# Kernel tuning notes

Measured on AMD Instinct MI355X. Metric: run time of the kernel, lower is better.

The kernel has to match this reference:

```python
import jax, jax.numpy as jnp
import numpy as np

V = 17  # number of skeleton joints (hard-coded in the torch module)
NUM_SUBSET = 3

def _dam_mask():
    # Reproduces the Python masking loops: zero block [12:17,12:17] and rows/cols {3,6,7,9,10}
    m = np.ones((V, V), np.float32)
    m[12:17, 12:17] = 0.0
    for j in (3, 6, 7, 9, 10):
        m[j, :] = 0.0
        m[:, j] = 0.0
    return jnp.asarray(m)

def setup_inputs() -> dict:
    key = jax.random.key(0)
    ks = jax.random.split(key, 8)
    N, Cin, Cout, T, G = 64, 64, 64, 256, 8
    return {
        "x": jax.random.normal(ks[0], (N, Cin, T, V), jnp.float32),
        "A_base": jax.random.uniform(ks[1], (NUM_SUBSET, V, V), jnp.float32),  # fixed adjacency buffer
        "DA": 0.01 * jax.random.normal(ks[2], (NUM_SUBSET, G, V, V), jnp.float32),   # DecoupleA param
        "DAM": 0.01 * jax.random.normal(ks[3], (NUM_SUBSET, G, V, V), jnp.float32),  # DecoupleAM param (masked, detached)
        "conv_w": jax.random.normal(ks[4], (NUM_SUBSET * Cout, Cin), jnp.float32) * (2.0 / Cin) ** 0.5,  # 1x1 conv
        "conv_b": jnp.zeros((NUM_SUBSET * Cout,), jnp.float32),
        "se_w": jax.random.normal(ks[5], (3,), jnp.float32) * 0.5,  # conv2_1: Conv1d(1,1,k=3,pad=1,no bias)
        "bn_gamma": jnp.full((Cout,), 1e-6, jnp.float32),  # bn_init(bn, 1e-6)
        "bn_beta": jnp.zeros((Cout,), jnp.float32),
    }

def reference(x, A_base, DA, DAM, conv_w, conv_b, se_w, bn_gamma, bn_beta):
    G = DA.shape[1]
    Cout = bn_gamma.shape[0]
    N, Cin, T, _ = x.shape
    # --- adjacency assembly: A (buffer, broadcast over groups) + DecoupleA + masked DecoupleAM ---
    A = A_base[:, None] + DA + DAM * _dam_mask()              # [3, G, V, V]
    # torch .repeat(1, out//groups, 1, 1) tiles along channel axis; + 0.04 from A_final loop
    A_final = jnp.tile(A, (1, Cout // G, 1, 1)) + 0.04        # [3, Cout, V, V]
    # --- 1x1 conv C_in -> 3*C_out ---
    m = jnp.einsum('nctv,kc->nktv', x, conv_w) + conv_b[None, :, None, None]
    m = m.reshape(N, NUM_SUBSET, Cout, T, V)
    # --- grouped adjacency aggregation (A_final has no batch dependence) ---
    m = jnp.einsum('nkctv,kcvw->nctw', m, A_final)            # [N, Cout, T, V]
    # --- SE-style channel attention: global avg pool -> Conv1d(k=3) over channels -> sigmoid gate ---
    p = m.mean(axis=(2, 3))                                   # [N, Cout]
    pp = jnp.pad(p, ((0, 0), (1, 1)))
    g = se_w[0] * pp[:, :-2] + se_w[1] * pp[:, 1:-1] + se_w[2] * pp[:, 2:]
    q = m + m * jax.nn.sigmoid(g)[:, :, None, None]
    # --- BatchNorm2d (training mode: batch stats over N,T,V) ---
    mu = q.mean(axis=(0, 2, 3), keepdims=True)
    var = q.var(axis=(0, 2, 3), keepdims=True)
    q = bn_gamma[None, :, None, None] * (q - mu) * jax.lax.rsqrt(var + 1e-5) + bn_beta[None, :, None, None]
    # --- residual (down == identity since in_channels == out_channels) and ReLU ---
    return jax.nn.relu(q + x)
```

## Files before the change

### kernel.cpp

```cpp
#include <hip/hip_runtime.h>
#include <math.h>

#define NN 64
#define CIN 64
#define COUT 64
#define TT 256
#define VV 17
#define NSUB 3
#define GG 8

#define WS_MB 0
#define WS_WBF 12288
#define WS_PSUM 18432
#define WS_SSQ 22528
#define WS_ACOEF 0
#define WS_BCOEF 4096
#define M2_BYTE_OFF 131072ull
#define M2F8_NEED (M2_BYTE_OFF + 1ull * 64 * 64 * 256 * 17)

typedef short bh8 __attribute__((ext_vector_type(8)));
typedef float f32x4 __attribute__((ext_vector_type(4)));
typedef float f32x16 __attribute__((ext_vector_type(16)));
typedef unsigned short u16t;

__device__ __forceinline__ unsigned bf16r(float f) {
    unsigned u = __builtin_bit_cast(unsigned, f);
    return (u + 0x7fffu + ((u >> 16) & 1u)) >> 16;
}
__device__ __forceinline__ float bf2f(unsigned us) {
    return __builtin_bit_cast(float, us << 16);
}

__device__ __forceinline__ float mfull(const float* Ab, const float* DA, const float* DAM,
                                       int s, int g, int v, int w) {
    const unsigned bad = (1u << 3) | (1u << 6) | (1u << 7) | (1u << 9) | (1u << 10);
    float mask = ((v >= 12 && w >= 12) || ((bad >> v) & 1) || ((bad >> w) & 1)) ? 0.f : 1.f;
    int src = ((s * GG + g) * VV + v) * VV + w;
    return Ab[(s * VV + v) * VV + w] + DA[src] + DAM[src] * mask + 0.04f;
}

__global__ void gcn_prep(const float* __restrict__ Ab, const float* __restrict__ DA,
                         const float* __restrict__ DAM, const float* __restrict__ convw,
                         float* __restrict__ ws) {
    int t0 = blockIdx.x * 256 + threadIdx.x;
    int stride = gridDim.x * 256;
    u16t* wbf = (u16t*)(ws + WS_WBF);
    for (int i = t0; i < 192 * 64; i += stride) wbf[i] = (u16t)bf16r(convw[i]);
    u16t* mb = (u16t*)(ws + WS_MB);
    for (int i = t0; i < NSUB * GG * 32 * 32; i += stride) {
        int k = i & 31, w = (i >> 5) & 31, g = (i >> 10) & 7, s = i >> 13;
        u16t val = 0;
        if (w < VV && k < VV) val = (u16t)bf16r(mfull(Ab, DA, DAM, s, g, k, w));
        mb[i] = val;
    }
}

template <int F8OUT>
__global__ __launch_bounds__(512, 4) void gcn_pass1(const float* __restrict__ x,
                                                    const float* __restrict__ convb,
                                                    const float* __restrict__ ws,
                                                    float* __restrict__ out,
                                                    unsigned char* __restrict__ m2f8) {
    __shared__ __align__(16) unsigned char smem[73984];
    u16t* xsT = (u16t*)smem;
    u16t* Wl = (u16t*)(smem + 20736);
    u16t* mt = (u16t*)(smem + 48384);

    const int tid = threadIdx.x;
    const int wv = tid >> 6;
    const int l = tid & 63;
    const int c16 = l & 15;
    const int q4 = (l >> 4) & 3;
    const int c32 = l & 31;
    const int hi = l >> 5;
    const int n = blockIdx.x >> 3;

    {
        const unsigned* wsrc = (const unsigned*)(ws + WS_WBF);
        unsigned* wd = (unsigned*)Wl;
        for (int j = tid; j < 192 * 32; j += 512) wd[(j >> 5) * 36 + (j & 31)] = wsrc[j];
        unsigned* mz = (unsigned*)mt;
        for (int j = tid; j < 6400; j += 512) mz[j] = 0u;
    }

    const u16t* mb16 = (const u16t*)(ws + WS_MB);
    const int madj = (wv * 32 + c32) * 32;

    for (int k4 = 0; k4 < 4; ++k4) {
        const int tt = (blockIdx.x & 7) * 4 + k4;

        const float* xb = x + (size_t)n * 278528 + tt * 136;
        for (int task = tid; task < 1088; task += 512) {
            int oct = task / 136;
            int col = task - 136 * oct;
            const float* src = xb + (8 * oct) * 4352 + col;
            uint4 pk;
            pk.x = bf16r(src[0]) | (bf16r(src[4352]) << 16);
            pk.y = bf16r(src[2 * 4352]) | (bf16r(src[3 * 4352]) << 16);
            pk.z = bf16r(src[4 * 4352]) | (bf16r(src[5 * 4352]) << 16);
            pk.w = bf16r(src[6 * 4352]) | (bf16r(src[7 * 4352]) << 16);
            *(uint4*)&((unsigned*)xsT)[col * 36 + oct * 4] = pk;
        }
        __syncthreads();

        f32x16 D2[2];
        D2[0] = 0; D2[1] = 0;

        const int colm = 16 * wv + c16;
        const int tm = (colm * 241) >> 12;
        const int offm = tm * 24 + (colm - 17 * tm);

#pragma unroll
        for (int s = 0; s < 3; ++s) {
            bh8 Bc0 = *(const bh8*)&xsT[colm * 72 + 8 * q4];
            bh8 Bc1 = *(const bh8*)&xsT[colm * 72 + 32 + 8 * q4];
            f32x4 Dc0 = *(const f32x4*)(convb + s * 64 + 4 * q4);
            f32x4 Dc1 = *(const f32x4*)(convb + s * 64 + 16 + 4 * q4);
            {
                bh8 A;
                A = *(const bh8*)&Wl[(s * 64 + c16) * 72 + 8 * q4];
                Dc0 = __builtin_amdgcn_mfma_f32_16x16x32_bf16(A, Bc0, Dc0, 0, 0, 0);
                A = *(const bh8*)&Wl[(s * 64 + c16) * 72 + 32 + 8 * q4];
                Dc0 = __builtin_amdgcn_mfma_f32_16x16x32_bf16(A, Bc1, Dc0, 0, 0, 0);
                A = *(const bh8*)&Wl[(s * 64 + 16 + c16) * 72 + 8 * q4];
                Dc1 = __builtin_amdgcn_mfma_f32_16x16x32_bf16(A, Bc0, Dc1, 0, 0, 0);
                A = *(const bh8*)&Wl[(s * 64 + 16 + c16) * 72 + 32 + 8 * q4];
                Dc1 = __builtin_amdgcn_mfma_f32_16x16x32_bf16(A, Bc1, Dc1, 0, 0, 0);
            }

            if (s > 0) __syncthreads();
#pragma unroll
            for (int i = 0; i < 4; ++i) {
                mt[(4 * q4 + i) * 200 + offm] = (u16t)bf16r(Dc0[i]);
                mt[(16 + 4 * q4 + i) * 200 + offm] = (u16t)bf16r(Dc1[i]);
            }

            Dc0 = *(const f32x4*)(convb + s * 64 + 32 + 4 * q4);
            Dc1 = *(const f32x4*)(convb + s * 64 + 48 + 4 * q4);
            {
                bh8 A;
                A = *(const bh8*)&Wl[(s * 64 + 32 + c16) * 72 + 8 * q4];
                Dc0 = __builtin_amdgcn_mfma_f32_16x16x32_bf16(A, Bc0, Dc0, 0, 0, 0);
                A = *(const bh8*)&Wl[(s * 64 + 32 + c16) * 72 + 32 + 8 * q4];
                Dc0 = __builtin_amdgcn_mfma_f32_16x16x32_bf16(A, Bc1, Dc0, 0, 0, 0);
                A = *(const bh8*)&Wl[(s * 64 + 48 + c16) * 72 + 8 * q4];
                Dc1 = __builtin_amdgcn_mfma_f32_16x16x32_bf16(A, Bc0, Dc1, 0, 0, 0);
                A = *(const bh8*)&Wl[(s * 64 + 48 + c16) * 72 + 32 + 8 * q4];
                Dc1 = __builtin_amdgcn_mfma_f32_16x16x32_bf16(A, Bc1, Dc1, 0, 0, 0);
            }
#pragma unroll
            for (int i = 0; i < 4; ++i) {
                mt[(32 + 4 * q4 + i) * 200 + offm] = (u16t)bf16r(Dc0[i]);
                mt[(48 + 4 * q4 + i) * 200 + offm] = (u16t)bf16r(Dc1[i]);
            }

            if (wv < 4) {
                f32x4 Dc8 = *(const f32x4*)(convb + s * 64 + 16 * wv + 4 * q4);
                bh8 B80 = *(const bh8*)&xsT[(128 + c16) * 72 + 8 * q4];
                bh8 B81 = *(const bh8*)&xsT[(128 + c16) * 72 + 32 + 8 * q4];
                bh8 A0 = *(const bh8*)&Wl[(s * 64 + 16 * wv + c16) * 72 + 8 * q4];
                bh8 A1 = *(const bh8*)&Wl[(s * 64 + 16 * wv + c16) * 72 + 32 + 8 * q4];
                Dc8 = __builtin_amdgcn_mfma_f32_16x16x32_bf16(A0, B80, Dc8, 0, 0, 0);
                Dc8 = __builtin_amdgcn_mfma_f32_16x16x32_bf16(A1, B81, Dc8, 0, 0, 0);
                if (c16 < 8) {
                    int off8 = 7 * 24 + (9 + c16);
                    int co0 = 16 * wv + 4 * q4;
#pragma unroll
                    for (int i = 0; i < 4; ++i)
                        mt[(co0 + i) * 200 + off8] = (u16t)bf16r(Dc8[i]);
                }
            }

            bh8 Bs = *(const bh8*)&mb16[s * 8192 + madj + 8 * hi];
            u16t mv16 = mb16[s * 8192 + madj + 16];
            __syncthreads();

            bh8 b2 = {0, 0, 0, 0, 0, 0, 0, 0};
            b2[0] = hi ? (short)0 : (short)mv16;

#pragma unroll
            for (int p = 0; p < 2; ++p) {
                int co = wv + 8 * ((c32 >> 3) + 4 * p);
                int base = co * 200 + (c32 & 7) * 24 + 8 * hi;
                bh8 a0 = *(const bh8*)&mt[base];
                bh8 a1 = *(const bh8*)&mt[base + 16];
                D2[p] = __builtin_amdgcn_mfma_f32_32x32x16_bf16(a0, Bs, D2[p], 0, 0, 0);
                D2[p] = __builtin_amdgcn_mfma_f32_32x32x16_bf16(a1, b2, D2[p], 0, 0, 0);
            }
        }

        u16t* stg = xsT;
#pragma unroll
        for (int p = 0; p < 2; ++p)
#pragma unroll
            for (int reg = 0; reg < 16; ++reg) {
                const int cosel = reg >> 2;
                const int t = (reg & 3) + 4 * hi;
                const int co = wv + 8 * (cosel + 4 * p);
                if (c32 < 17) stg[co * 144 + t * 17 + c32] = (u16t)bf16r(D2[p][reg]);
            }
        __syncthreads();

        if (F8OUT) {
            unsigned char* gm = m2f8 + (size_t)(n * 32 + tt) * 8704;
#pragma unroll
            for (int it = 0; it < 3; ++it) {
                int c = tid + 512 * it;
                if (c < 1088) {
                    int co = c / 17, j = c - 17 * co;
                    uint4 u = *(const uint4*)&stg[co * 144 + 8 * j];
                    float f0 = bf2f(u.x & 0xffffu), f1 = bf2f(u.x >> 16);
                    float f2 = bf2f(u.y & 0xffffu), f3 = bf2f(u.y >> 16);
                    float f4 = bf2f(u.z & 0xffffu), f5 = bf2f(u.z >> 16);
                    float f6 = bf2f(u.w & 0xffffu), f7 = bf2f(u.w >> 16);
                    int lo = __builtin_amdgcn_cvt_pk_fp8_f32(f0, f1, 0, false);
                    lo = __builtin_amdgcn_cvt_pk_fp8_f32(f2, f3, lo, true);
                    int hi2 = __builtin_amdgcn_cvt_pk_fp8_f32(f4, f5, 0, false);
                    hi2 = __builtin_amdgcn_cvt_pk_fp8_f32(f6, f7, hi2, true);
                    uint2 o;
                    o.x = (unsigned)lo;
                    o.y = (unsigned)hi2;
                    *(uint2*)(gm + 8 * c) = o;
                }
            }
        } else {
            float* ob = out + (size_t)n * 278528 + tt * 136;
#pragma unroll
            for (int it = 0; it < 5; ++it) {
                int c = tid + 512 * it;
                if (c < 2176) {
                    int co = c / 34;
                    int pos = c - 34 * co;
                    uint2 u = *(const uint2*)&stg[co * 144 + pos * 4];
                    float4 v;
                    v.x = bf2f(u.x & 0xffffu);
                    v.y = bf2f(u.x >> 16);
                    v.z = bf2f(u.y & 0xffffu);
                    v.w = bf2f(u.y >> 16);
                    *(float4*)(ob + co * 4352 + pos * 4) = v;
                }
            }
        }
        __syncthreads();
    }
}

__device__ __forceinline__ void block_reduce2(float& s1, float& s2, float* r1, float* r2,
                                              int tid) {
#pragma unroll
    for (int m = 1; m < 64; m <<= 1) {
        s1 += __shfl_xor(s1, m);
        s2 += __shfl_xor(s2, m);
    }
    int wv = tid >> 6;
    if ((tid & 63) == 0) { r1[wv] = s1; r2[wv] = s2; }
    __syncthreads();
    if (tid == 0) {
        s1 = r1[0] + r1[1] + r1[2] + r1[3];
        s2 = r2[0] + r2[1] + r2[2] + r2[3];
    }
}

__global__ __launch_bounds__(256) void gcn_colsum_f8(const unsigned char* __restrict__ m2f8,
                                                     float* __restrict__ psum,
                                                     float* __restrict__ ssq) {
    const int n = blockIdx.x >> 6, co = blockIdx.x & 63;
    const int tid = threadIdx.x;
    __shared__ float r1[4], r2[4];
    float s1 = 0.f, s2 = 0.f;
    for (int slot = tid; slot < 544; slot += 256) {
        int tt = slot / 17, i = slot - 17 * tt;
        const unsigned char* p = m2f8 + (size_t)(n * 32 + tt) * 8704 + co * 136 + i * 8;
        uint2 u = *(const uint2*)p;
        float f0 = __builtin_amdgcn_cvt_f32_fp8((int)u.x, 0);
        float f1 = __builtin_amdgcn_cvt_f32_fp8((int)u.x, 1);
        float f2 = __builtin_amdgcn_cvt_f32_fp8((int)u.x, 2);
        float f3 = __builtin_amdgcn_cvt_f32_fp8((int)u.x, 3);
        float f4 = __builtin_amdgcn_cvt_f32_fp8((int)u.y, 0);
        float f5 = __builtin_amdgcn_cvt_f32_fp8((int)u.y, 1);
        float f6 = __builtin_amdgcn_cvt_f32_fp8((int)u.y, 2);
        float f7 = __builtin_amdgcn_cvt_f32_fp8((int)u.y, 3);
        s1 += ((f0 + f1) + (f2 + f3)) + ((f4 + f5) + (f6 + f7));
        s2 += fmaf(f0, f0, fmaf(f1, f1, fmaf(f2, f2, f3 * f3))) +
              fmaf(f4, f4, fmaf(f5, f5, fmaf(f6, f6, f7 * f7)));
    }
    block_reduce2(s1, s2, r1, r2, tid);
    if (tid == 0) {
        psum[n * 64 + co] = s1;
        ssq[n * 64 + co] = s2;
    }
}

__global__ __launch_bounds__(256) void gcn_colsum_f32(const float* __restrict__ m2,
                                                      float* __restrict__ psum,
                                                      float* __restrict__ ssq) {
    const int n = blockIdx.x >> 6, co = blockIdx.x & 63;
    const int tid = threadIdx.x;
    __shared__ float r1[4], r2[4];
    float s1 = 0.f, s2 = 0.f;
    const float4* p = (const float4*)(m2 + (size_t)n * 278528 + co * 4352);
    for (int u = tid; u < 1088; u += 256) {
        float4 v = p[u];
        s1 += v.x + v.y + v.z + v.w;
        s2 += v.x * v.x + v.y * v.y + v.z * v.z + v.w * v.w;
    }
    block_reduce2(s1, s2, r1, r2, tid);
    if (tid == 0) {
        psum[n * 64 + co] = s1;
        ssq[n * 64 + co] = s2;
    }
}

__global__ void gcn_stats(const float* __restrict__ se_w, const float* __restrict__ gamma,
                          const float* __restrict__ beta, float* __restrict__ ws) {
    __shared__ float ps[4096], sc[4096], q2s[4096];
    __shared__ float mu_s[64], inv_s[64];
    int tid = threadIdx.x;
    const float* psum = ws + WS_PSUM;
    const float* ssq = ws + WS_SSQ;
    float* acoef = ws + WS_ACOEF;
    float* bcoef = ws + WS_BCOEF;
    for (int i = tid; i < 4096; i += 256) ps[i] = psum[i] * (1.f / (TT * VV));
    __syncthreads();
    float w0 = se_w[0], w1 = se_w[1], w2 = se_w[2];
    for (int i = tid; i < 4096; i += 256) {
        int c = i & 63;
        float pm = (c > 0) ? ps[i - 1] : 0.f;
        float pp = (c < 63) ? ps[i + 1] : 0.f;
        float gg = w0 * pm + w1 * ps[i] + w2 * pp;
        float s = 1.f + 1.f / (1.f + expf(-gg));
        sc[i] = s;
        q2s[i] = s * s * ssq[i];
    }
    __syncthreads();
    if (tid < 64) {
        float mu = 0.f, e2 = 0.f;
        for (int nn = 0; nn < 64; ++nn) {
            mu += sc[nn * 64 + tid] * ps[nn * 64 + tid];
            e2 += q2s[nn * 64 + tid];
        }
        mu *= (1.f / 64.f);
        e2 *= (1.f / (64.f * TT * VV));
        float var = e2 - mu * mu;
        mu_s[tid] = mu;
        inv_s[tid] = rsqrtf(var + 1e-5f);
    }
    __syncthreads();
    for (int i = tid; i < 4096; i += 256) {
        int c = i & 63;
        float gin = gamma[c] * inv_s[c];
        acoef[i] = gin * sc[i];
        bcoef[i] = beta[c] - gin * mu_s[c];
    }
}

__global__ __launch_bounds__(256) void gcn_final_f32(const float* __restrict__ x,
                                                     const float* __restrict__ ws,
                                                     float* __restrict__ out) {
    const float* acoef = ws + WS_ACOEF;
    const float* bcoef = ws + WS_BCOEF;
    int i = blockIdx.x * 256 + threadIdx.x;
    const int total4 = (NN * COUT * TT * VV) / 4;
    if (i >= total4) return;
    int nc = i / ((TT * VV) / 4);
    float a = acoef[nc], b = bcoef[nc];
    float4 m = ((const float4*)out)[i];
    float4 xx = ((const float4*)x)[i];
    float4 r;
    r.x = fmaxf(fmaf(a, m.x, b) + xx.x, 0.f);
    r.y = fmaxf(fmaf(a, m.y, b) + xx.y, 0.f);
    r.z = fmaxf(fmaf(a, m.z, b) + xx.z, 0.f);
    r.w = fmaxf(fmaf(a, m.w, b) + xx.w, 0.f);
    ((float4*)out)[i] = r;
}

__global__ __launch_bounds__(256) void gcn_final_f8(const float* __restrict__ x,
                                                    const float* __restrict__ ws,
                                                    const unsigned char* __restrict__ m2f8,
                                                    float* __restrict__ out) {
    const float* acoef = ws + WS_ACOEF;
    const float* bcoef = ws + WS_BCOEF;
    const int bt = blockIdx.x;
    const int n = bt >> 5, tt = bt & 31;
    const unsigned char* gm = m2f8 + (size_t)bt * 8704;
    const size_t base = (size_t)n * 278528 + tt * 136;
    const int tid = threadIdx.x;
#pragma unroll
    for (int it = 0; it < 5; ++it) {
        int task = tid + 256 * it;
        if (task < 1088) {
            int co = task / 17, j = task - 17 * co;
            float a = acoef[n * 64 + co], b = bcoef[n * 64 + co];
            uint2 u = *(const uint2*)(gm + 8 * task);
            float m0 = __builtin_amdgcn_cvt_f32_fp8((int)u.x, 0);
            float m1 = __builtin_amdgcn_cvt_f32_fp8((int)u.x, 1);
            float m2v = __builtin_amdgcn_cvt_f32_fp8((int)u.x, 2);
            float m3 = __builtin_amdgcn_cvt_f32_fp8((int)u.x, 3);
            float m4 = __builtin_amdgcn_cvt_f32_fp8((int)u.y, 0);
            float m5 = __builtin_amdgcn_cvt_f32_fp8((int)u.y, 1);
            float m6 = __builtin_amdgcn_cvt_f32_fp8((int)u.y, 2);
            float m7 = __builtin_amdgcn_cvt_f32_fp8((int)u.y, 3);
            const float* xp = x + base + co * 4352 + 8 * j;
            float4 x0 = *(const float4*)xp;
            float4 x1 = *(const float4*)(xp + 4);
            float4 r0, r1;
            r0.x = fmaxf(fmaf(a, m0, b) + x0.x, 0.f);
            r0.y = fmaxf(fmaf(a, m1, b) + x0.y, 0.f);
            r0.z = fmaxf(fmaf(a, m2v, b) + x0.z, 0.f);
            r0.w = fmaxf(fmaf(a, m3, b) + x0.w, 0.f);
            r1.x = fmaxf(fmaf(a, m4, b) + x1.x, 0.f);
            r1.y = fmaxf(fmaf(a, m5, b) + x1.y, 0.f);
            r1.z = fmaxf(fmaf(a, m6, b) + x1.z, 0.f);
            r1.w = fmaxf(fmaf(a, m7, b) + x1.w, 0.f);
            float* op = out + base + co * 4352 + 8 * j;
            *(float4*)op = r0;
            *(float4*)(op + 4) = r1;
        }
    }
}

extern "C" void kernel_launch(void* const* d_in, const int* in_sizes, int n_in,
                              void* d_out, int out_size, void* d_ws, size_t ws_size,
                              hipStream_t stream) {
    const float* x = (const float*)d_in[0];
    const float* Ab = (const float*)d_in[1];
    const float* DA = (const float*)d_in[2];
    const float* DAM = (const float*)d_in[3];
    const float* convw = (const float*)d_in[4];
    const float* convb = (const float*)d_in[5];
    const float* sew = (const float*)d_in[6];
    const float* gamma = (const float*)d_in[7];
    const float* beta = (const float*)d_in[8];
    float* out = (float*)d_out;
    float* ws = (float*)d_ws;
    unsigned char* m2f8 = (unsigned char*)d_ws + M2_BYTE_OFF;
    const bool f8path = ws_size >= M2F8_NEED;

    gcn_prep<<<16, 256, 0, stream>>>(Ab, DA, DAM, convw, ws);
    if (f8path) {
        gcn_pass1<1><<<512, 512, 0, stream>>>(x, convb, ws, out, m2f8);
        gcn_colsum_f8<<<4096, 256, 0, stream>>>(m2f8, ws + WS_PSUM, ws + WS_SSQ);
        gcn_stats<<<1, 256, 0, stream>>>(sew, gamma, beta, ws);
        gcn_final_f8<<<2048, 256, 0, stream>>>(x, ws, m2f8, out);
    } else {
        gcn_pass1<0><<<512, 512, 0, stream>>>(x, convb, ws, out, m2f8);
        gcn_colsum_f32<<<4096, 256, 0, stream>>>(out, ws + WS_PSUM, ws + WS_SSQ);
        gcn_stats<<<1, 256, 0, stream>>>(sew, gamma, beta, ws);
        const int total4 = (NN * COUT * TT * VV) / 4;
        gcn_final_f32<<<(total4 + 255) / 256, 256, 0, stream>>>(x, ws, out);
    }
}
```

Before: 106.9 us.

## Double-buffer conv output tile in LDS and read conv weights from global

Splits the shared conv-output tile into two ping-pong buffers selected by subset parity, so the barrier before each subset's writes can be dropped. The staged bf16 conv weights are no longer copied into LDS; A fragments are loaded directly from the global workspace instead, which frees LDS for the second buffer. This removes one barrier per subset and the weight staging copy, at the cost of per-MFMA global/L1 loads of weights and a larger zero-initialisation.

New measurement: 185.9 us. 73.9% more time.

```diff
diff --git a/kernel.cpp b/kernel.cpp
--- a/kernel.cpp
+++ b/kernel.cpp
@@ -61,10 +61,10 @@
                                                     const float* __restrict__ ws,
                                                     float* __restrict__ out,
                                                     unsigned char* __restrict__ m2f8) {
-    __shared__ __align__(16) unsigned char smem[73984];
+    __shared__ __align__(16) unsigned char smem[71936];
     u16t* xsT = (u16t*)smem;
-    u16t* Wl = (u16t*)(smem + 20736);
-    u16t* mt = (u16t*)(smem + 48384);
+    u16t* mt0 = (u16t*)(smem + 20736);
+    u16t* mt1 = (u16t*)(smem + 46336);
 
     const int tid = threadIdx.x;
     const int wv = tid >> 6;
@@ -76,14 +76,12 @@
     const int n = blockIdx.x >> 3;
 
     {
-        const unsigned* wsrc = (const unsigned*)(ws + WS_WBF);
-        unsigned* wd = (unsigned*)Wl;
-        for (int j = tid; j < 192 * 32; j += 512) wd[(j >> 5) * 36 + (j & 31)] = wsrc[j];
-        unsigned* mz = (unsigned*)mt;
-        for (int j = tid; j < 6400; j += 512) mz[j] = 0u;
+        unsigned* mz = (unsigned*)mt0;
+        for (int j = tid; j < 12800; j += 512) mz[j] = 0u;
     }
 
     const u16t* mb16 = (const u16t*)(ws + WS_MB);
+    const u16t* wbf = (const u16t*)(ws + WS_WBF);
     const int madj = (wv * 32 + c32) * 32;
 
     for (int k4 = 0; k4 < 4; ++k4) {
@@ -112,54 +110,54 @@
 
 #pragma unroll
         for (int s = 0; s < 3; ++s) {
+            u16t* mts = (s & 1) ? mt1 : mt0;
+
             bh8 Bc0 = *(const bh8*)&xsT[colm * 72 + 8 * q4];
             bh8 Bc1 = *(const bh8*)&xsT[colm * 72 + 32 + 8 * q4];
             f32x4 Dc0 = *(const f32x4*)(convb + s * 64 + 4 * q4);
             f32x4 Dc1 = *(const f32x4*)(convb + s * 64 + 16 + 4 * q4);
             {
                 bh8 A;
-                A = *(const bh8*)&Wl[(s * 64 + c16) * 72 + 8 * q4];
+                A = *(const bh8*)&wbf[(s * 64 + c16) * 64 + 8 * q4];
                 Dc0 = __builtin_amdgcn_mfma_f32_16x16x32_bf16(A, Bc0, Dc0, 0, 0, 0);
-                A = *(const bh8*)&Wl[(s * 64 + c16) * 72 + 32 + 8 * q4];
+                A = *(const bh8*)&wbf[(s * 64 + c16) * 64 + 32 + 8 * q4];
                 Dc0 = __builtin_amdgcn_mfma_f32_16x16x32_bf16(A, Bc1, Dc0, 0, 0, 0);
-                A = *(const bh8*)&Wl[(s * 64 + 16 + c16) * 72 + 8 * q4];
+                A = *(const bh8*)&wbf[(s * 64 + 16 + c16) * 64 + 8 * q4];
                 Dc1 = __builtin_amdgcn_mfma_f32_16x16x32_bf16(A, Bc0, Dc1, 0, 0, 0);
-                A = *(const bh8*)&Wl[(s * 64 + 16 + c16) * 72 + 32 + 8 * q4];
+                A = *(const bh8*)&wbf[(s * 64 + 16 + c16) * 64 + 32 + 8 * q4];
                 Dc1 = __builtin_amdgcn_mfma_f32_16x16x32_bf16(A, Bc1, Dc1, 0, 0, 0);
             }
-
-            if (s > 0) __syncthreads();
 #pragma unroll
             for (int i = 0; i < 4; ++i) {
-                mt[(4 * q4 + i) * 200 + offm] = (u16t)bf16r(Dc0[i]);
-                mt[(16 + 4 * q4 + i) * 200 + offm] = (u16t)bf16r(Dc1[i]);
+                mts[(4 * q4 + i) * 200 + offm] = (u16t)bf16r(Dc0[i]);
+                mts[(16 + 4 * q4 + i) * 200 + offm] = (u16t)bf16r(Dc1[i]);
             }
 
             Dc0 = *(const f32x4*)(convb + s * 64 + 32 + 4 * q4);
             Dc1 = *(const f32x4*)(convb + s * 64 + 48 + 4 * q4);
             {
                 bh8 A;
-                A = *(const bh8*)&Wl[(s * 64 + 32 + c16) * 72 + 8 * q4];
+                A = *(const bh8*)&wbf[(s * 64 + 32 + c16) * 64 + 8 * q4];
                 Dc0 = __builtin_amdgcn_mfma_f32_16x16x32_bf16(A, Bc0, Dc0, 0, 0, 0);
-                A = *(const bh8*)&Wl[(s * 64 + 32 + c16) * 72 + 32 + 8 * q4];
+                A = *(const bh8*)&wbf[(s * 64 + 32 + c16) * 64 + 32 + 8 * q4];
                 Dc0 = __builtin_amdgcn_mfma_f32_16x16x32_bf16(A, Bc1, Dc0, 0, 0, 0);
-                A = *(const bh8*)&Wl[(s * 64 + 48 + c16) * 72 + 8 * q4];
+                A = *(const bh8*)&wbf[(s * 64 + 48 + c16) * 64 + 8 * q4];
                 Dc1 = __builtin_amdgcn_mfma_f32_16x16x32_bf16(A, Bc0, Dc1, 0, 0, 0);
-                A = *(const bh8*)&Wl[(s * 64 + 48 + c16) * 72 + 32 + 8 * q4];
+                A = *(const bh8*)&wbf[(s * 64 + 48 + c16) * 64 + 32 + 8 * q4];
                 Dc1 = __builtin_amdgcn_mfma_f32_16x16x32_bf16(A, Bc1, Dc1, 0, 0, 0);
             }
 #pragma unroll
             for (int i = 0; i < 4; ++i) {
-                mt[(32 + 4 * q4 + i) * 200 + offm] = (u16t)bf16r(Dc0[i]);
-                mt[(48 + 4 * q4 + i) * 200 + offm] = (u16t)bf16r(Dc1[i]);
+                mts[(32 + 4 * q4 + i) * 200 + offm] = (u16t)bf16r(Dc0[i]);
+                mts[(48 + 4 * q4 + i) * 200 + offm] = (u16t)bf16r(Dc1[i]);
             }
 
             if (wv < 4) {
                 f32x4 Dc8 = *(const f32x4*)(convb + s * 64 + 16 * wv + 4 * q4);
                 bh8 B80 = *(const bh8*)&xsT[(128 + c16) * 72 + 8 * q4];
                 bh8 B81 = *(const bh8*)&xsT[(128 + c16) * 72 + 32 + 8 * q4];
-                bh8 A0 = *(const bh8*)&Wl[(s * 64 + 16 * wv + c16) * 72 + 8 * q4];
-                bh8 A1 = *(const bh8*)&Wl[(s * 64 + 16 * wv + c16) * 72 + 32 + 8 * q4];
+                bh8 A0 = *(const bh8*)&wbf[(s * 64 + 16 * wv + c16) * 64 + 8 * q4];
+                bh8 A1 = *(const bh8*)&wbf[(s * 64 + 16 * wv + c16) * 64 + 32 + 8 * q4];
                 Dc8 = __builtin_amdgcn_mfma_f32_16x16x32_bf16(A0, B80, Dc8, 0, 0, 0);
                 Dc8 = __builtin_amdgcn_mfma_f32_16x16x32_bf16(A1, B81, Dc8, 0, 0, 0);
                 if (c16 < 8) {
@@ -167,7 +165,7 @@
                     int co0 = 16 * wv + 4 * q4;
 #pragma unroll
                     for (int i = 0; i < 4; ++i)
-                        mt[(co0 + i) * 200 + off8] = (u16t)bf16r(Dc8[i]);
+                        mts[(co0 + i) * 200 + off8] = (u16t)bf16r(Dc8[i]);
                 }
             }
 
@@ -182,8 +180,8 @@
             for (int p = 0; p < 2; ++p) {
                 int co = wv + 8 * ((c32 >> 3) + 4 * p);
                 int base = co * 200 + (c32 & 7) * 24 + 8 * hi;
-                bh8 a0 = *(const bh8*)&mt[base];
-                bh8 a1 = *(const bh8*)&mt[base + 16];
+                bh8 a0 = *(const bh8*)&mts[base];
+                bh8 a1 = *(const bh8*)&mts[base + 16];
                 D2[p] = __builtin_amdgcn_mfma_f32_32x32x16_bf16(a0, Bs, D2[p], 0, 0, 0);
                 D2[p] = __builtin_amdgcn_mfma_f32_32x32x16_bf16(a1, b2, D2[p], 0, 0, 0);
             }
```
